# Kernel tuning notes

Hardware: AMD Instinct MI355X
Metric: run time of the kernel (lower is better)

Reference implementation:

```python
import jax, jax.numpy as jnp
import numpy as np

# --- CT geometry (stand-in for ctlib `options`): parallel-beam Radon transform ---
H = 256; W = 256          # image size
V = 192                   # number of projection views
D = 256                   # detector bins
S = 256                   # samples along each ray
_SQ2 = float(np.sqrt(2.0))
_ANG = jnp.asarray(np.linspace(0.0, np.pi, V, endpoint=False), jnp.float32)      # view angles
_DET = jnp.asarray(np.linspace(-_SQ2, _SQ2, D), jnp.float32)                      # detector coords (world units, image in [-1,1]^2)
_T   = jnp.asarray(np.linspace(-_SQ2, _SQ2, S), jnp.float32)                      # sample positions along ray
_DT  = jnp.float32(2.0 * _SQ2 / S)                                                # ray step length


def _bilerp(img, xp, yp):
    """Bilinear gather from img [H,W] at pixel coords xp,yp; zero outside."""
    x0 = jnp.floor(xp); y0 = jnp.floor(yp)
    ix0 = x0.astype(jnp.int32); iy0 = y0.astype(jnp.int32)
    fx = xp - x0; fy = yp - y0
    def gat(ix, iy):
        valid = (ix >= 0) & (ix < W) & (iy >= 0) & (iy < H)
        v = img[jnp.clip(iy, 0, H - 1), jnp.clip(ix, 0, W - 1)]
        return jnp.where(valid, v, jnp.float32(0.0))
    return (gat(ix0, iy0) * (1 - fx) * (1 - fy)
            + gat(ix0 + 1, iy0) * fx * (1 - fy)
            + gat(ix0, iy0 + 1) * (1 - fx) * fy
            + gat(ix0 + 1, iy0 + 1) * fx * fy)


def project2d(img):
    """Ray-driven forward projection: img [H,W] -> sinogram [V,D]."""
    cos = jnp.cos(_ANG)[:, None, None]; sin = jnp.sin(_ANG)[:, None, None]
    s = _DET[None, :, None]; t = _T[None, None, :]
    # world coords of sample points along each ray: [V,D,S]
    xw = -s * sin + t * cos
    yw = s * cos + t * sin
    # world [-1,1] -> pixel coords
    xp = (xw + 1.0) * (W / 2.0) - 0.5
    yp = (yw + 1.0) * (H / 2.0) - 0.5
    return _bilerp(img, xp, yp).sum(-1) * _DT


def backproject2d(sino):
    """Exact adjoint of project2d (ray-driven scatter): [V,D] -> [H,W]."""
    _, vjp_fn = jax.vjp(project2d, jnp.zeros((H, W), sino.dtype))
    return vjp_fn(sino)[0]


def setup_inputs() -> dict:
    key = jax.random.key(0)
    k1, k2, k3 = jax.random.split(key, 3)
    input_data = jax.random.normal(k1, (2, 1, H, W), jnp.float32)
    proj = jax.random.normal(k2, (2, 1, V, D), jnp.float32)
    weight = jax.random.uniform(k3, (1,), jnp.float32)
    return {"input_data": input_data, "proj": proj, "weight": weight}


def reference(input_data, proj, weight):
    B, C = input_data.shape[:2]
    imgs = input_data.reshape(B * C, H, W)
    sino = jax.vmap(project2d)(imgs).reshape(proj.shape)          # A x
    temp = sino - proj                                            # A x - p
    ir = jax.vmap(backproject2d)(temp.reshape(B * C, V, D)).reshape(input_data.shape)  # A^T (A x - p)
    return input_data - weight * ir
```

## Files before the change

### kernel.cpp

```cpp
#include <hip/hip_runtime.h>
#include <math.h>

#define HH 256
#define WW 256
#define VV 192
#define DD 256

#define DSQ2      1.41421356237309504880
#define F_DT      ((float)(2.0 * DSQ2 / 256.0))
#define F_INV_DS  ((float)(255.0 / (2.0 * DSQ2)))
#define F_SIG     ((float)(256.0 * DSQ2 / 255.0))
#define F_RAD     ((float)(128.0 * DSQ2))

#define TPITCH 67
#define NSEG 16
#define NV (VV / NSEG)

static __device__ __forceinline__ float view_angle(int v) {
    return (float)((double)v * (3.14159265358979323846 / 192.0));
}

__global__ __launch_bounds__(256)
void init_kernel(const float* __restrict__ input,
                 float* __restrict__ out,
                 float* __restrict__ sacc,
                 int npix4, int nsino4) {
    const int stride = gridDim.x * 256;
    const float4* in4 = (const float4*)input;
    float4* o4 = (float4*)out;
    float4* s4 = (float4*)sacc;
    for (int i = blockIdx.x * 256 + threadIdx.x; i < npix4; i += stride)
        o4[i] = in4[i];
    for (int i = blockIdx.x * 256 + threadIdx.x; i < nsino4; i += stride)
        s4[i] = make_float4(0.f, 0.f, 0.f, 0.f);
}

__global__ __launch_bounds__(256)
void fwd_tile_kernel(const float* __restrict__ img_all,
                     float* __restrict__ sacc) {
    __shared__ float tile[66 * TPITCH];
    const int tx = (blockIdx.x & 3) << 6;
    const int ty = (blockIdx.x >> 2) << 6;
    const int v  = blockIdx.y;
    const int b  = blockIdx.z;
    const int tid  = threadIdx.x;
    const int lane = tid & 63;
    const int wv   = tid >> 6;

    const float* __restrict__ img = img_all + (b << 16);

    for (int k = tid; k < 64 * 16; k += 256) {
        const int r  = k >> 4;
        const int c4 = (k & 15) << 2;
        const float4 val = *(const float4*)(img + ((ty + r) << 8) + tx + c4);
        float* dst = tile + (r + 1) * TPITCH + 1 + c4;
        dst[0] = val.x; dst[1] = val.y; dst[2] = val.z; dst[3] = val.w;
    }
    if (tid < 132) {
        const int r  = tid >> 1;
        const int cc = (tid & 1) ? 65 : 0;
        const int gx = tx - 1 + cc;
        const int gy = ty - 1 + r;
        float vv = 0.0f;
        if ((unsigned)gx < 256u && (unsigned)gy < 256u) vv = img[(gy << 8) + gx];
        tile[r * TPITCH + cc] = vv;
    }
    if (tid < 128) {
        const int cc = 1 + (tid & 63);
        const int r  = (tid >> 6) ? 65 : 0;
        const int gx = tx - 1 + cc;
        const int gy = ty - 1 + r;
        float vv = 0.0f;
        if ((unsigned)gx < 256u && (unsigned)gy < 256u) vv = img[(gy << 8) + gx];
        tile[r * TPITCH + cc] = vv;
    }

    float sn, cs;
    sincosf(view_angle(v), &sn, &cs);
    const float Xd = -sn * F_SIG, Yd = cs * F_SIG;
    const float Xt =  cs * F_SIG, Yt = sn * F_SIG;
    const float X0 = 127.5f - F_RAD * (cs - sn);
    const float Y0 = 127.5f - F_RAD * (cs + sn);

    const int lox = (tx == 0) ? -1 : 0;
    const int loy = (ty == 0) ? -1 : 0;
    const unsigned spanx = (unsigned)(64 - lox);
    const unsigned spany = (unsigned)(64 - loy);

    const float xwl = ((float)(tx + lox) + 0.5f) * (1.0f / 128.0f) - 1.0f;
    const float xwh = ((float)(tx + 64)  + 0.5f) * (1.0f / 128.0f) - 1.0f;
    const float ywl = ((float)(ty + loy) + 0.5f) * (1.0f / 128.0f) - 1.0f;
    const float ywh = ((float)(ty + 64)  + 0.5f) * (1.0f / 128.0f) - 1.0f;
    const float dA = -xwl * sn, dB = -xwh * sn;
    const float dC =  ywl * cs, dDq =  ywh * cs;
    const float tAq =  xwl * cs, tB =  xwh * cs;
    const float tC =  ywl * sn, tD =  ywh * sn;
    const float dcmin = 127.5f + (fminf(dA, dB) + fminf(dC, dDq)) * F_INV_DS;
    const float dcmax = 127.5f + (fmaxf(dA, dB) + fmaxf(dC, dDq)) * F_INV_DS;
    const float tcmin = 127.5f + (fminf(tAq, tB) + fminf(tC, tD)) * F_INV_DS;
    const float tcmax = 127.5f + (fmaxf(tAq, tB) + fmaxf(tC, tD)) * F_INV_DS;
    const int dlo = max(0, (int)ceilf(dcmin - 0.002f));
    const int dhi = min(255, (int)floorf(dcmax + 0.002f));
    const int tlo = max(0, (int)ceilf(tcmin - 0.002f));
    const int thi = min(255, (int)floorf(tcmax + 0.002f));

    __syncthreads();

    const int sbase = (b * VV + v) << 8;
    for (int dbase = dlo; dbase <= dhi; dbase += 64) {
        const int d = dbase + lane;
        float acc = 0.0f;
        float xc = fmaf((float)d, Xd, fmaf((float)(tlo + wv), Xt, X0)) - (float)tx + 1.0f;
        float yc = fmaf((float)d, Yd, fmaf((float)(tlo + wv), Yt, Y0)) - (float)ty + 1.0f;
        const float step_x = 4.0f * Xt, step_y = 4.0f * Yt;
#pragma unroll 2
        for (int t = tlo + wv; t <= thi; t += 4) {
            const float xf = floorf(xc);
            const float yf = floorf(yc);
            const int cx = (int)xf;
            const int cy = (int)yf;
            const float fx = xc - xf;
            const float fy = yc - yf;
            const bool ok = (((unsigned)(cx - 1 - lox) < spanx) &
                             ((unsigned)(cy - 1 - loy) < spany));
            const int cxc = min(max(cx, 0), 65);
            const int cyc = min(max(cy, 0), 64);
            const float* p = tile + cyc * TPITCH + cxc;
            const float v00 = p[0],      v10 = p[1];
            const float v01 = p[TPITCH], v11 = p[TPITCH + 1];
            const float top = fmaf(fx, v10 - v00, v00);
            const float bot = fmaf(fx, v11 - v01, v01);
            const float smp = fmaf(fy, bot - top, top);
            acc += ok ? smp : 0.0f;
            xc += step_x; yc += step_y;
        }
        if (acc != 0.0f && d <= dhi)
            atomicAdd(sacc + sbase + d, acc);
    }
}

__global__ __launch_bounds__(256, 8)
void bwd_partial_kernel(const float* __restrict__ sacc,
                        const float* __restrict__ proj,
                        const float* __restrict__ weight,
                        float* __restrict__ out) {
    __shared__ float s_t[NV * DD];
    __shared__ float4 s_g[NV];
    const int tid = threadIdx.x;
    const int v0 = blockIdx.y * NV;
    const int b  = (int)blockIdx.x >> 7;

    if (tid < NV) {
        float sn, cs;
        sincosf(view_angle(v0 + tid), &sn, &cs);
        s_g[tid] = make_float4(cs, sn, F_SIG * cs, F_SIG * sn);
    }
    {
        const int base = (b * VV + v0) << 8;
        const float4* s4 = (const float4*)(sacc + base);
        const float4* p4 = (const float4*)(proj + base);
#pragma unroll
        for (int k = 0; k < NV * (DD / 4) / 256; ++k) {
            const int i = tid + (k << 8);
            const float4 a = s4[i];
            const float4 p = p4[i];
            float4 r;
            r.x = fmaf(F_DT, a.x, -p.x);
            r.y = fmaf(F_DT, a.y, -p.y);
            r.z = fmaf(F_DT, a.z, -p.z);
            r.w = fmaf(F_DT, a.w, -p.w);
            ((float4*)s_t)[i] = r;
        }
    }
    __syncthreads();

    const int idx = ((int)blockIdx.x << 9) + tid;
    const int y0 = (idx >> 8) & 255;
    const int x  = idx & 255;
    const float xw  = (float)x  * (1.0f / 128.0f) + (0.5f / 128.0f - 1.0f);
    const float yw0 = (float)y0 * (1.0f / 128.0f) + (0.5f / 128.0f - 1.0f);
    const float yw1 = yw0 + (1.0f / 128.0f);

    float acc0 = 0.0f, acc1 = 0.0f;
#pragma unroll 2
    for (int vi = 0; vi < NV; ++vi) {
        const float4 g = s_g[vi];
        const float* __restrict__ row = s_t + (vi << 8);
#pragma unroll
        for (int p = 0; p < 2; ++p) {
            const float yw = p ? yw1 : yw0;
            const float sw = fmaf(-xw, g.y, yw * g.x);
            const float tw = fmaf( xw, g.x, yw * g.y);
            const float dc = fmaf(sw, F_INV_DS, 127.5f);
            const float tc = fmaf(tw, F_INV_DS, 127.5f);
            const float d0f = floorf(dc);
            const float t0f = floorf(tc);
            const int d0 = (int)d0f;
            const float fd = dc - d0f;
            const float ft = tc - t0f;

            const float dx00 = fmaf(g.z, -ft, g.w * fd);
            const float dyn  = fmaf(g.z,  fd, g.w * ft);
            const float dx01 = dx00 + g.z;
            const float dy01 = g.w - dyn;
            const float dx10 = dx00 - g.w;
            const float dy10 = g.z - dyn;
            const float dx11 = dx01 - g.w;
            const float dy11 = dy10 + g.w;

            const float w00 = fmaxf(0.0f, 1.0f - fabsf(dx00)) * fmaxf(0.0f, 1.0f - fabsf(dyn));
            const float w01 = fmaxf(0.0f, 1.0f - fabsf(dx01)) * fmaxf(0.0f, 1.0f - fabsf(dy01));
            const float w10 = fmaxf(0.0f, 1.0f - fabsf(dx10)) * fmaxf(0.0f, 1.0f - fabsf(dy10));
            const float w11 = fmaxf(0.0f, 1.0f - fabsf(dx11)) * fmaxf(0.0f, 1.0f - fabsf(dy11));

            const float rA = row[d0];
            const float rB = row[d0 + 1];
            if (p == 0) {
                acc0 = fmaf(w00 + w01, rA, acc0);
                acc0 = fmaf(w10 + w11, rB, acc0);
            } else {
                acc1 = fmaf(w00 + w01, rA, acc1);
                acc1 = fmaf(w10 + w11, rB, acc1);
            }
        }
    }

    const float c = -weight[0] * F_DT;
    atomicAdd(out + idx, c * acc0);
    atomicAdd(out + idx + 256, c * acc1);
}

extern "C" void kernel_launch(void* const* d_in, const int* in_sizes, int n_in,
                              void* d_out, int out_size, void* d_ws, size_t ws_size,
                              hipStream_t stream) {
    const float* input  = (const float*)d_in[0];
    const float* proj   = (const float*)d_in[1];
    const float* weight = (const float*)d_in[2];
    float* out  = (float*)d_out;
    float* sacc = (float*)d_ws;

    const int nb = in_sizes[0] / (HH * WW);
    const int npix = nb * HH * WW;

    init_kernel<<<256, 256, 0, stream>>>(input, out, sacc,
                                         npix / 4, nb * VV * DD / 4);
    fwd_tile_kernel<<<dim3(16, VV, nb), 256, 0, stream>>>(input, sacc);
    bwd_partial_kernel<<<dim3(npix / 512, NSEG), 256, 0, stream>>>(sacc, proj, weight, out);
}
```

Before: 101.8 us.

## Process four pixel rows per thread in backprojection and fold input copy into forward

The backprojection kernel now gives each thread four vertically adjacent pixels instead of two and advances the detector and ray coordinates by a precomputed per-view increment instead of recomputing them, so each staged sinogram tile is shared by more pixels per block. The copy of the input image into the output moves from the init kernel into the view-0 blocks of the forward kernel, leaving init to only zero the sinogram accumulator. The forward sampling loop is unrolled by 4 instead of 2. The trade-offs are half as many backprojection blocks, more registers per thread, and incremental coordinate updates that may accumulate float rounding differently.

```diff
diff --git a/kernel.cpp b/kernel.cpp
--- a/kernel.cpp
+++ b/kernel.cpp
@@ -9,6 +9,7 @@
 #define DSQ2      1.41421356237309504880
 #define F_DT      ((float)(2.0 * DSQ2 / 256.0))
 #define F_INV_DS  ((float)(255.0 / (2.0 * DSQ2)))
+#define F_DDY     ((float)(255.0 / (2.0 * DSQ2) / 128.0))
 #define F_SIG     ((float)(256.0 * DSQ2 / 255.0))
 #define F_RAD     ((float)(128.0 * DSQ2))
 
@@ -21,23 +22,17 @@
 }
 
 __global__ __launch_bounds__(256)
-void init_kernel(const float* __restrict__ input,
-                 float* __restrict__ out,
-                 float* __restrict__ sacc,
-                 int npix4, int nsino4) {
-    const int stride = gridDim.x * 256;
-    const float4* in4 = (const float4*)input;
-    float4* o4 = (float4*)out;
-    float4* s4 = (float4*)sacc;
-    for (int i = blockIdx.x * 256 + threadIdx.x; i < npix4; i += stride)
-        o4[i] = in4[i];
-    for (int i = blockIdx.x * 256 + threadIdx.x; i < nsino4; i += stride)
-        s4[i] = make_float4(0.f, 0.f, 0.f, 0.f);
+void init_kernel(float* __restrict__ sacc, int nsino4) {
+    const int i = blockIdx.x * 256 + threadIdx.x;
+    if (i < nsino4)
+        ((float4*)sacc)[i] = make_float4(0.f, 0.f, 0.f, 0.f);
 }
 
 __global__ __launch_bounds__(256)
 void fwd_tile_kernel(const float* __restrict__ img_all,
-                     float* __restrict__ sacc) {
+                     float* __restrict__ sacc,
+                     float* __restrict__ out,
+                     int npix4) {
     __shared__ float tile[66 * TPITCH];
     const int tx = (blockIdx.x & 3) << 6;
     const int ty = (blockIdx.x >> 2) << 6;
@@ -46,6 +41,17 @@
     const int tid  = threadIdx.x;
     const int lane = tid & 63;
     const int wv   = tid >> 6;
+
+    if (v == 0) {
+        const int chunk = (b << 4) + blockIdx.x;
+        const float4* in4 = (const float4*)img_all;
+        float4* o4 = (float4*)out;
+#pragma unroll
+        for (int k = 0; k < 4; ++k) {
+            const int i = (chunk << 10) + (k << 8) + tid;
+            if (i < npix4) o4[i] = in4[i];
+        }
+    }
 
     const float* __restrict__ img = img_all + (b << 16);
 
@@ -113,7 +119,7 @@
         float xc = fmaf((float)d, Xd, fmaf((float)(tlo + wv), Xt, X0)) - (float)tx + 1.0f;
         float yc = fmaf((float)d, Yd, fmaf((float)(tlo + wv), Yt, Y0)) - (float)ty + 1.0f;
         const float step_x = 4.0f * Xt, step_y = 4.0f * Yt;
-#pragma unroll 2
+#pragma unroll 4
         for (int t = tlo + wv; t <= thi; t += 4) {
             const float xf = floorf(xc);
             const float yf = floorf(yc);
@@ -146,14 +152,16 @@
                         float* __restrict__ out) {
     __shared__ float s_t[NV * DD];
     __shared__ float4 s_g[NV];
+    __shared__ float2 s_gd[NV];
     const int tid = threadIdx.x;
     const int v0 = blockIdx.y * NV;
-    const int b  = (int)blockIdx.x >> 7;
+    const int b  = (int)blockIdx.x >> 6;
 
     if (tid < NV) {
         float sn, cs;
         sincosf(view_angle(v0 + tid), &sn, &cs);
-        s_g[tid] = make_float4(cs, sn, F_SIG * cs, F_SIG * sn);
+        s_g[tid]  = make_float4(cs, sn, F_SIG * cs, F_SIG * sn);
+        s_gd[tid] = make_float2(F_DDY * cs, F_DDY * sn);
     }
     {
         const int base = (b * VV + v0) << 8;
@@ -174,25 +182,24 @@
     }
     __syncthreads();
 
-    const int idx = ((int)blockIdx.x << 9) + tid;
+    const int idx = ((int)blockIdx.x << 10) + tid;
     const int y0 = (idx >> 8) & 255;
     const int x  = idx & 255;
     const float xw  = (float)x  * (1.0f / 128.0f) + (0.5f / 128.0f - 1.0f);
     const float yw0 = (float)y0 * (1.0f / 128.0f) + (0.5f / 128.0f - 1.0f);
-    const float yw1 = yw0 + (1.0f / 128.0f);
-
-    float acc0 = 0.0f, acc1 = 0.0f;
+
+    float acc[4] = {0.f, 0.f, 0.f, 0.f};
 #pragma unroll 2
     for (int vi = 0; vi < NV; ++vi) {
-        const float4 g = s_g[vi];
+        const float4 g  = s_g[vi];
+        const float2 gd = s_gd[vi];
         const float* __restrict__ row = s_t + (vi << 8);
-#pragma unroll
-        for (int p = 0; p < 2; ++p) {
-            const float yw = p ? yw1 : yw0;
-            const float sw = fmaf(-xw, g.y, yw * g.x);
-            const float tw = fmaf( xw, g.x, yw * g.y);
-            const float dc = fmaf(sw, F_INV_DS, 127.5f);
-            const float tc = fmaf(tw, F_INV_DS, 127.5f);
+        const float sw = fmaf(-xw, g.y, yw0 * g.x);
+        const float tw = fmaf( xw, g.x, yw0 * g.y);
+        float dc = fmaf(sw, F_INV_DS, 127.5f);
+        float tc = fmaf(tw, F_INV_DS, 127.5f);
+#pragma unroll
+        for (int k = 0; k < 4; ++k) {
             const float d0f = floorf(dc);
             const float t0f = floorf(tc);
             const int d0 = (int)d0f;
@@ -213,21 +220,16 @@
             const float w10 = fmaxf(0.0f, 1.0f - fabsf(dx10)) * fmaxf(0.0f, 1.0f - fabsf(dy10));
             const float w11 = fmaxf(0.0f, 1.0f - fabsf(dx11)) * fmaxf(0.0f, 1.0f - fabsf(dy11));
 
-            const float rA = row[d0];
-            const float rB = row[d0 + 1];
-            if (p == 0) {
-                acc0 = fmaf(w00 + w01, rA, acc0);
-                acc0 = fmaf(w10 + w11, rB, acc0);
-            } else {
-                acc1 = fmaf(w00 + w01, rA, acc1);
-                acc1 = fmaf(w10 + w11, rB, acc1);
-            }
+            acc[k] = fmaf(w00 + w01, row[d0],     acc[k]);
+            acc[k] = fmaf(w10 + w11, row[d0 + 1], acc[k]);
+            dc += gd.x; tc += gd.y;
         }
     }
 
     const float c = -weight[0] * F_DT;
-    atomicAdd(out + idx, c * acc0);
-    atomicAdd(out + idx + 256, c * acc1);
+#pragma unroll
+    for (int k = 0; k < 4; ++k)
+        atomicAdd(out + idx + (k << 8), c * acc[k]);
 }
 
 extern "C" void kernel_launch(void* const* d_in, const int* in_sizes, int n_in,
@@ -241,9 +243,9 @@
 
     const int nb = in_sizes[0] / (HH * WW);
     const int npix = nb * HH * WW;
-
-    init_kernel<<<256, 256, 0, stream>>>(input, out, sacc,
-                                         npix / 4, nb * VV * DD / 4);
-    fwd_tile_kernel<<<dim3(16, VV, nb), 256, 0, stream>>>(input, sacc);
-    bwd_partial_kernel<<<dim3(npix / 512, NSEG), 256, 0, stream>>>(sacc, proj, weight, out);
-}
+    const int nsino4 = nb * VV * DD / 4;
+
+    init_kernel<<<(nsino4 + 255) / 256, 256, 0, stream>>>(sacc, nsino4);
+    fwd_tile_kernel<<<dim3(16, VV, nb), 256, 0, stream>>>(input, sacc, out, npix / 4);
+    bwd_partial_kernel<<<dim3(npix / 1024, NSEG), 256, 0, stream>>>(sacc, proj, weight, out);
+}
```

After: 103.3 us. No clear change (+1.4%).

## Halve forward tile height, fold image copy into forward kernel, simplify tile addressing

Applied to the files above, without the earlier changes.

The forward projection tile shrinks from 64x64 to 64x32 pixels, doubling the block count and cutting shared memory per block. This gives more parallelism and a tighter ray-bound range per block, at the cost of more atomics and more per-block setup. The input-to-output copy moves from the init kernel into the v==0 blocks of the forward kernel, so init only zeroes the sinogram accumulator. The bilinear address clamp becomes a single select on the in-bounds flag, and the inner loop unroll goes from 2 to 4.

```diff
diff --git a/kernel.cpp b/kernel.cpp
--- a/kernel.cpp
+++ b/kernel.cpp
@@ -13,6 +13,7 @@
 #define F_RAD     ((float)(128.0 * DSQ2))
 
 #define TPITCH 67
+#define TROWS  34
 #define NSEG 16
 #define NV (VV / NSEG)
 
@@ -21,42 +22,47 @@
 }
 
 __global__ __launch_bounds__(256)
-void init_kernel(const float* __restrict__ input,
-                 float* __restrict__ out,
-                 float* __restrict__ sacc,
-                 int npix4, int nsino4) {
-    const int stride = gridDim.x * 256;
-    const float4* in4 = (const float4*)input;
-    float4* o4 = (float4*)out;
-    float4* s4 = (float4*)sacc;
-    for (int i = blockIdx.x * 256 + threadIdx.x; i < npix4; i += stride)
-        o4[i] = in4[i];
-    for (int i = blockIdx.x * 256 + threadIdx.x; i < nsino4; i += stride)
-        s4[i] = make_float4(0.f, 0.f, 0.f, 0.f);
+void init_kernel(float* __restrict__ sacc, int nsino4) {
+    const int i = blockIdx.x * 256 + threadIdx.x;
+    if (i < nsino4)
+        ((float4*)sacc)[i] = make_float4(0.f, 0.f, 0.f, 0.f);
 }
 
 __global__ __launch_bounds__(256)
 void fwd_tile_kernel(const float* __restrict__ img_all,
-                     float* __restrict__ sacc) {
-    __shared__ float tile[66 * TPITCH];
+                     float* __restrict__ sacc,
+                     float* __restrict__ out,
+                     int npix4) {
+    __shared__ float tile[TROWS * TPITCH];
     const int tx = (blockIdx.x & 3) << 6;
-    const int ty = (blockIdx.x >> 2) << 6;
+    const int ty = (blockIdx.x >> 2) << 5;
     const int v  = blockIdx.y;
     const int b  = blockIdx.z;
     const int tid  = threadIdx.x;
     const int lane = tid & 63;
     const int wv   = tid >> 6;
 
+    if (v == 0) {
+        const int chunk = (b << 5) + blockIdx.x;
+        const float4* in4 = (const float4*)img_all;
+        float4* o4 = (float4*)out;
+#pragma unroll
+        for (int k = 0; k < 2; ++k) {
+            const int i = (chunk << 9) + (k << 8) + tid;
+            if (i < npix4) o4[i] = in4[i];
+        }
+    }
+
     const float* __restrict__ img = img_all + (b << 16);
 
-    for (int k = tid; k < 64 * 16; k += 256) {
+    for (int k = tid; k < 32 * 16; k += 256) {
         const int r  = k >> 4;
         const int c4 = (k & 15) << 2;
         const float4 val = *(const float4*)(img + ((ty + r) << 8) + tx + c4);
         float* dst = tile + (r + 1) * TPITCH + 1 + c4;
         dst[0] = val.x; dst[1] = val.y; dst[2] = val.z; dst[3] = val.w;
     }
-    if (tid < 132) {
+    if (tid < 68) {
         const int r  = tid >> 1;
         const int cc = (tid & 1) ? 65 : 0;
         const int gx = tx - 1 + cc;
@@ -67,7 +73,7 @@
     }
     if (tid < 128) {
         const int cc = 1 + (tid & 63);
-        const int r  = (tid >> 6) ? 65 : 0;
+        const int r  = (tid >> 6) ? 33 : 0;
         const int gx = tx - 1 + cc;
         const int gy = ty - 1 + r;
         float vv = 0.0f;
@@ -85,12 +91,12 @@
     const int lox = (tx == 0) ? -1 : 0;
     const int loy = (ty == 0) ? -1 : 0;
     const unsigned spanx = (unsigned)(64 - lox);
-    const unsigned spany = (unsigned)(64 - loy);
+    const unsigned spany = (unsigned)(32 - loy);
 
     const float xwl = ((float)(tx + lox) + 0.5f) * (1.0f / 128.0f) - 1.0f;
     const float xwh = ((float)(tx + 64)  + 0.5f) * (1.0f / 128.0f) - 1.0f;
     const float ywl = ((float)(ty + loy) + 0.5f) * (1.0f / 128.0f) - 1.0f;
-    const float ywh = ((float)(ty + 64)  + 0.5f) * (1.0f / 128.0f) - 1.0f;
+    const float ywh = ((float)(ty + 32)  + 0.5f) * (1.0f / 128.0f) - 1.0f;
     const float dA = -xwl * sn, dB = -xwh * sn;
     const float dC =  ywl * cs, dDq =  ywh * cs;
     const float tAq =  xwl * cs, tB =  xwh * cs;
@@ -113,7 +119,7 @@
         float xc = fmaf((float)d, Xd, fmaf((float)(tlo + wv), Xt, X0)) - (float)tx + 1.0f;
         float yc = fmaf((float)d, Yd, fmaf((float)(tlo + wv), Yt, Y0)) - (float)ty + 1.0f;
         const float step_x = 4.0f * Xt, step_y = 4.0f * Yt;
-#pragma unroll 2
+#pragma unroll 4
         for (int t = tlo + wv; t <= thi; t += 4) {
             const float xf = floorf(xc);
             const float yf = floorf(yc);
@@ -123,9 +129,8 @@
             const float fy = yc - yf;
             const bool ok = (((unsigned)(cx - 1 - lox) < spanx) &
                              ((unsigned)(cy - 1 - loy) < spany));
-            const int cxc = min(max(cx, 0), 65);
-            const int cyc = min(max(cy, 0), 64);
-            const float* p = tile + cyc * TPITCH + cxc;
+            const int addr = ok ? (cy * TPITCH + cx) : 0;
+            const float* p = tile + addr;
             const float v00 = p[0],      v10 = p[1];
             const float v01 = p[TPITCH], v11 = p[TPITCH + 1];
             const float top = fmaf(fx, v10 - v00, v00);
@@ -241,9 +246,9 @@
 
     const int nb = in_sizes[0] / (HH * WW);
     const int npix = nb * HH * WW;
-
-    init_kernel<<<256, 256, 0, stream>>>(input, out, sacc,
-                                         npix / 4, nb * VV * DD / 4);
-    fwd_tile_kernel<<<dim3(16, VV, nb), 256, 0, stream>>>(input, sacc);
+    const int nsino4 = nb * VV * DD / 4;
+
+    init_kernel<<<(nsino4 + 255) / 256, 256, 0, stream>>>(sacc, nsino4);
+    fwd_tile_kernel<<<dim3(32, VV, nb), 256, 0, stream>>>(input, sacc, out, npix / 4);
     bwd_partial_kernel<<<dim3(npix / 512, NSEG), 256, 0, stream>>>(sacc, proj, weight, out);
 }
```

New measurement: 110.1 us. +8.1%, slower.

## Clip forward rays per detector to the tile and process two views per block

Applied to the files above, without the earlier changes.

The forward tile kernel now works out, for each detector ray, the exact interval of sample steps that crosses the 64x64 tile (slab intersection), so it stops walking empty samples. Work is remapped so that 16 detectors per wave are each split across 4 sample phases, with the partial sums combined by cross-lane shuffles before one atomic per detector. Each block now handles two views, which halves how often the tile is loaded from global memory. An extra zero row is added so the clamp on tile addressing can be dropped. The cost is more per-ray setup, reduced lane parallelism over detectors, and less balanced loop trip counts across lanes.

```diff
diff --git a/kernel.cpp b/kernel.cpp
--- a/kernel.cpp
+++ b/kernel.cpp
@@ -13,11 +13,28 @@
 #define F_RAD     ((float)(128.0 * DSQ2))
 
 #define TPITCH 67
+#define TROWS  67
 #define NSEG 16
 #define NV (VV / NSEG)
+#define VG 2
 
 static __device__ __forceinline__ float view_angle(int v) {
     return (float)((double)v * (3.14159265358979323846 / 192.0));
+}
+
+static __device__ __forceinline__ void axis_interval(float L, float lo, float hi,
+                                                     float step, float& a, float& b) {
+    if (fabsf(step) > 1e-5f) {
+        const float r = 1.0f / step;
+        const float u = (lo - L) * r;
+        const float w = (hi - L) * r;
+        a = fminf(u, w);
+        b = fmaxf(u, w);
+    } else {
+        const bool in = (L >= lo) && (L < hi);
+        a = in ? -1e9f : 1e9f;
+        b = in ?  1e9f : -1e9f;
+    }
 }
 
 __global__ __launch_bounds__(256)
@@ -38,14 +55,16 @@
 __global__ __launch_bounds__(256)
 void fwd_tile_kernel(const float* __restrict__ img_all,
                      float* __restrict__ sacc) {
-    __shared__ float tile[66 * TPITCH];
+    __shared__ float tile[TROWS * TPITCH];
     const int tx = (blockIdx.x & 3) << 6;
     const int ty = (blockIdx.x >> 2) << 6;
-    const int v  = blockIdx.y;
+    const int v0 = blockIdx.y * VG;
     const int b  = blockIdx.z;
     const int tid  = threadIdx.x;
     const int lane = tid & 63;
     const int wv   = tid >> 6;
+    const int doff = lane & 15;
+    const int ph   = lane >> 4;
 
     const float* __restrict__ img = img_all + (b << 16);
 
@@ -74,68 +93,88 @@
         if ((unsigned)gx < 256u && (unsigned)gy < 256u) vv = img[(gy << 8) + gx];
         tile[r * TPITCH + cc] = vv;
     }
-
-    float sn, cs;
-    sincosf(view_angle(v), &sn, &cs);
-    const float Xd = -sn * F_SIG, Yd = cs * F_SIG;
-    const float Xt =  cs * F_SIG, Yt = sn * F_SIG;
-    const float X0 = 127.5f - F_RAD * (cs - sn);
-    const float Y0 = 127.5f - F_RAD * (cs + sn);
+    if (tid < TPITCH) tile[66 * TPITCH + tid] = 0.0f;
 
     const int lox = (tx == 0) ? -1 : 0;
     const int loy = (ty == 0) ? -1 : 0;
     const unsigned spanx = (unsigned)(64 - lox);
     const unsigned spany = (unsigned)(64 - loy);
-
-    const float xwl = ((float)(tx + lox) + 0.5f) * (1.0f / 128.0f) - 1.0f;
-    const float xwh = ((float)(tx + 64)  + 0.5f) * (1.0f / 128.0f) - 1.0f;
-    const float ywl = ((float)(ty + loy) + 0.5f) * (1.0f / 128.0f) - 1.0f;
-    const float ywh = ((float)(ty + 64)  + 0.5f) * (1.0f / 128.0f) - 1.0f;
-    const float dA = -xwl * sn, dB = -xwh * sn;
-    const float dC =  ywl * cs, dDq =  ywh * cs;
-    const float tAq =  xwl * cs, tB =  xwh * cs;
-    const float tC =  ywl * sn, tD =  ywh * sn;
-    const float dcmin = 127.5f + (fminf(dA, dB) + fminf(dC, dDq)) * F_INV_DS;
-    const float dcmax = 127.5f + (fmaxf(dA, dB) + fmaxf(dC, dDq)) * F_INV_DS;
-    const float tcmin = 127.5f + (fminf(tAq, tB) + fminf(tC, tD)) * F_INV_DS;
-    const float tcmax = 127.5f + (fmaxf(tAq, tB) + fmaxf(tC, tD)) * F_INV_DS;
-    const int dlo = max(0, (int)ceilf(dcmin - 0.002f));
-    const int dhi = min(255, (int)floorf(dcmax + 0.002f));
-    const int tlo = max(0, (int)ceilf(tcmin - 0.002f));
-    const int thi = min(255, (int)floorf(tcmax + 0.002f));
+    const float txl = (float)(tx + lox), txh = (float)(tx + 64);
+    const float tyl = (float)(ty + loy), tyh = (float)(ty + 64);
+    const float xwl = (txl + 0.5f) * (1.0f / 128.0f) - 1.0f;
+    const float xwh = (txh + 0.5f) * (1.0f / 128.0f) - 1.0f;
+    const float ywl = (tyl + 0.5f) * (1.0f / 128.0f) - 1.0f;
+    const float ywh = (tyh + 0.5f) * (1.0f / 128.0f) - 1.0f;
 
     __syncthreads();
 
-    const int sbase = (b * VV + v) << 8;
-    for (int dbase = dlo; dbase <= dhi; dbase += 64) {
-        const int d = dbase + lane;
-        float acc = 0.0f;
-        float xc = fmaf((float)d, Xd, fmaf((float)(tlo + wv), Xt, X0)) - (float)tx + 1.0f;
-        float yc = fmaf((float)d, Yd, fmaf((float)(tlo + wv), Yt, Y0)) - (float)ty + 1.0f;
-        const float step_x = 4.0f * Xt, step_y = 4.0f * Yt;
+    for (int vg = 0; vg < VG; ++vg) {
+        const int v = v0 + vg;
+        float sn, cs;
+        sincosf(view_angle(v), &sn, &cs);
+        const float Xd = -sn * F_SIG, Yd = cs * F_SIG;
+        const float Xt =  cs * F_SIG, Yt = sn * F_SIG;
+        const float X0 = 127.5f - F_RAD * (cs - sn);
+        const float Y0 = 127.5f - F_RAD * (cs + sn);
+
+        const float dA = -xwl * sn, dB = -xwh * sn;
+        const float dC =  ywl * cs, dDq =  ywh * cs;
+        const float tAq =  xwl * cs, tB =  xwh * cs;
+        const float tC =  ywl * sn, tD =  ywh * sn;
+        const float dcmin = 127.5f + (fminf(dA, dB) + fminf(dC, dDq)) * F_INV_DS;
+        const float dcmax = 127.5f + (fmaxf(dA, dB) + fmaxf(dC, dDq)) * F_INV_DS;
+        const float tcmin = 127.5f + (fminf(tAq, tB) + fminf(tC, tD)) * F_INV_DS;
+        const float tcmax = 127.5f + (fmaxf(tAq, tB) + fmaxf(tC, tD)) * F_INV_DS;
+        const int dlo = max(0, (int)ceilf(dcmin - 0.002f));
+        const int dhi = min(255, (int)floorf(dcmax + 0.002f));
+        const int tlo = max(0, (int)ceilf(tcmin - 0.002f));
+        const int thi = min(255, (int)floorf(tcmax + 0.002f));
+
+        const int sbase = (b * VV + v) << 8;
+        for (int dbase = dlo; dbase <= dhi; dbase += 64) {
+            const int d = dbase + (wv << 4) + doff;
+            const float xLg = fmaf((float)d, Xd, X0);
+            const float yLg = fmaf((float)d, Yd, Y0);
+
+            float ax, bx, ay, by;
+            axis_interval(xLg, txl, txh, Xt, ax, bx);
+            axis_interval(yLg, tyl, tyh, Yt, ay, by);
+            const float tminf = fmaxf(ax, ay);
+            const float tmaxf = fminf(bx, by);
+            const float tbf = fminf(fmaxf(tminf - 0.002f, (float)tlo), 300.0f);
+            const float tef = fmaxf(fminf(tmaxf + 0.002f, (float)thi), -2.0f);
+            int tb = (int)ceilf(tbf);
+            const int te = (int)floorf(tef);
+            tb += (ph - tb) & 3;
+
+            float acc = 0.0f;
+            float xc = fmaf((float)tb, Xt, xLg) - (float)tx + 1.0f;
+            float yc = fmaf((float)tb, Yt, yLg) - (float)ty + 1.0f;
+            const float sx = 4.0f * Xt, sy = 4.0f * Yt;
 #pragma unroll 2
-        for (int t = tlo + wv; t <= thi; t += 4) {
-            const float xf = floorf(xc);
-            const float yf = floorf(yc);
-            const int cx = (int)xf;
-            const int cy = (int)yf;
-            const float fx = xc - xf;
-            const float fy = yc - yf;
-            const bool ok = (((unsigned)(cx - 1 - lox) < spanx) &
-                             ((unsigned)(cy - 1 - loy) < spany));
-            const int cxc = min(max(cx, 0), 65);
-            const int cyc = min(max(cy, 0), 64);
-            const float* p = tile + cyc * TPITCH + cxc;
-            const float v00 = p[0],      v10 = p[1];
-            const float v01 = p[TPITCH], v11 = p[TPITCH + 1];
-            const float top = fmaf(fx, v10 - v00, v00);
-            const float bot = fmaf(fx, v11 - v01, v01);
-            const float smp = fmaf(fy, bot - top, top);
-            acc += ok ? smp : 0.0f;
-            xc += step_x; yc += step_y;
+            for (int t = tb; t <= te; t += 4) {
+                const float xf = floorf(xc);
+                const float yf = floorf(yc);
+                const int cx = (int)xf;
+                const int cy = (int)yf;
+                const float fx = xc - xf;
+                const float fy = yc - yf;
+                const bool ok = (((unsigned)(cx - 1 - lox) < spanx) &
+                                 ((unsigned)(cy - 1 - loy) < spany));
+                const int a0 = max(cy * TPITCH + cx, 0);
+                const float v00 = tile[a0],          v10 = tile[a0 + 1];
+                const float v01 = tile[a0 + TPITCH], v11 = tile[a0 + TPITCH + 1];
+                const float top = fmaf(fx, v10 - v00, v00);
+                const float bot = fmaf(fx, v11 - v01, v01);
+                const float smp = fmaf(fy, bot - top, top);
+                acc += ok ? smp : 0.0f;
+                xc += sx; yc += sy;
+            }
+            acc += __shfl_xor(acc, 16, 64);
+            acc += __shfl_xor(acc, 32, 64);
+            if (ph == 0 && acc != 0.0f && d <= dhi)
+                atomicAdd(sacc + sbase + d, acc);
         }
-        if (acc != 0.0f && d <= dhi)
-            atomicAdd(sacc + sbase + d, acc);
     }
 }
 
@@ -242,8 +281,7 @@
     const int nb = in_sizes[0] / (HH * WW);
     const int npix = nb * HH * WW;
 
-    init_kernel<<<256, 256, 0, stream>>>(input, out, sacc,
-                                         npix / 4, nb * VV * DD / 4);
-    fwd_tile_kernel<<<dim3(16, VV, nb), 256, 0, stream>>>(input, sacc);
+    init_kernel<<<256, 256, 0, stream>>>(input, out, sacc, npix / 4, nb * VV * DD / 4);
+    fwd_tile_kernel<<<dim3(16, VV / VG, nb), 256, 0, stream>>>(input, sacc);
     bwd_partial_kernel<<<dim3(npix / 512, NSEG), 256, 0, stream>>>(sacc, proj, weight, out);
 }
```

After: 98.76 us (median of 2 runs). 1.03x faster.
